# Performance work log

Hardware: AMD Instinct MI355X
Metric: run time of the kernel (lower is better)

The kernel has to match this reference:

```python
import math
import jax, jax.numpy as jnp
import numpy as np

N_HEADS = 8
WINDOW = 4


def _get_relative_embeddings(emb, length, window):
    # emb: [1, 2*window+1, k_channels] -> [1, 2*length-1, k_channels]
    pad_length = max(length - (window + 1), 0)
    start = max(window + 1 - length, 0)
    if pad_length > 0:
        emb = jnp.pad(emb, ((0, 0), (pad_length, pad_length), (0, 0)))
    return emb[:, start:start + 2 * length - 1]


def _relative_position_to_absolute_position(x):
    # x: [b, h, l, 2l-1] -> [b, h, l, l] (skewing trick)
    b, h, l, _ = x.shape
    x = jnp.pad(x, ((0, 0), (0, 0), (0, 0), (0, 1)))
    x_flat = x.reshape(b, h, l * 2 * l)
    x_flat = jnp.pad(x_flat, ((0, 0), (0, 0), (0, l - 1)))
    return x_flat.reshape(b, h, l + 1, 2 * l - 1)[:, :, :l, l - 1:]


def _absolute_position_to_relative_position(x):
    # x: [b, h, l, l] -> [b, h, l, 2l-1]
    b, h, l, _ = x.shape
    x = jnp.pad(x, ((0, 0), (0, 0), (0, 0), (0, l - 1)))
    x_flat = x.reshape(b, h, l * l + l * (l - 1))
    x_flat = jnp.pad(x_flat, ((0, 0), (0, 0), (l, 0)))
    return x_flat.reshape(b, h, l, 2 * l)[:, :, :, 1:]


def setup_inputs() -> dict:
    key = jax.random.key(0)
    ks = jax.random.split(key, 12)
    b, t, d = 4, 1024, 512
    kc = d // N_HEADS
    s = 1.0 / math.sqrt(d)
    return {
        "x": jax.random.normal(ks[0], (b, t, d), jnp.float32),
        "c": jax.random.normal(ks[1], (b, t, d), jnp.float32),
        "wq": jax.random.normal(ks[2], (d, d), jnp.float32) * s,
        "bq": jnp.zeros((d,), jnp.float32),
        "wk": jax.random.normal(ks[3], (d, d), jnp.float32) * s,
        "bk": jnp.zeros((d,), jnp.float32),
        "wv": jax.random.normal(ks[4], (d, d), jnp.float32) * s,
        "bv": jnp.zeros((d,), jnp.float32),
        "wo": jax.random.normal(ks[5], (d, d), jnp.float32) * s,
        "bo": jnp.zeros((d,), jnp.float32),
        "emb_rel_k": jax.random.normal(ks[6], (1, 2 * WINDOW + 1, kc), jnp.float32) * kc ** -0.5,
        "emb_rel_v": jax.random.normal(ks[7], (1, 2 * WINDOW + 1, kc), jnp.float32) * kc ** -0.5,
    }


def reference(x, c, wq, bq, wk, bk, wv, bv, wo, bo, emb_rel_k, emb_rel_v):
    b, t, d = x.shape
    h = N_HEADS
    kc = d // h
    inv_sqrt = 1.0 / math.sqrt(kc)

    # 1x1 conv projections (pointwise matmul)
    q = x @ wq + bq   # [b, t, d]
    k = c @ wk + bk
    v = c @ wv + bv

    # Faithful reshape as in source: [b, t, d] -> [b, h, kc, t] -> [b, h, t, kc]
    q = q.reshape(b, h, kc, t).transpose(0, 1, 3, 2)
    k = k.reshape(b, h, kc, t).transpose(0, 1, 3, 2)
    v = v.reshape(b, h, kc, t).transpose(0, 1, 3, 2)

    scores = jnp.einsum('bhtd,bhsd->bhts', q, k) * inv_sqrt  # [b,h,t,t]

    # relative key logits
    key_rel = _get_relative_embeddings(emb_rel_k, t, WINDOW)[0]  # [2t-1, kc]
    rel_logits = jnp.einsum('bhtd,md->bhtm', q, key_rel)          # [b,h,t,2t-1]
    scores_local = _relative_position_to_absolute_position(rel_logits) * inv_sqrt
    scores = scores + scores_local

    p_attn = jax.nn.softmax(scores, axis=-1)
    output = jnp.einsum('bhts,bhsd->bhtd', p_attn, v)  # [b,h,t,kc]

    # relative value contribution
    rel_weights = _absolute_position_to_relative_position(p_attn)  # [b,h,t,2t-1]
    val_rel = _get_relative_embeddings(emb_rel_v, t, WINDOW)[0]    # [2t-1, kc]
    output = output + jnp.einsum('bhtm,md->bhtd', rel_weights, val_rel)

    # Faithful output reshape: [b,h,t,kc] -> [b,h,kc,t] -> [b,t,d]
    output = output.transpose(0, 1, 3, 2).reshape(b, t, d)
    out = output @ wo + bo
    return out
```

## Files before the change

kernel.cpp:

```cpp
#include <hip/hip_runtime.h>
#include <hip/hip_bf16.h>

#define NB 4
#define NT 1024
#define ND 512
#define NH 8
#define NKC 64

typedef __bf16 bf16x8 __attribute__((ext_vector_type(8)));
typedef float f32x4 __attribute__((ext_vector_type(4)));
typedef unsigned int u32;

__device__ __forceinline__ f32x4 MFMA(bf16x8 a, bf16x8 b, f32x4 c) {
    return __builtin_amdgcn_mfma_f32_16x16x32_bf16(a, b, c, 0, 0, 0);
}
__device__ __forceinline__ unsigned short f2bu(float v) {
    __hip_bfloat16 b = __float2bfloat16(v);
    return *(unsigned short*)&b;
}
__device__ __forceinline__ void split1(float v, unsigned short& h, unsigned short& l)
{
    __hip_bfloat16 hb = __float2bfloat16(v);
    float r = v - __bfloat162float(hb);
    __hip_bfloat16 lb = __float2bfloat16(r);
    h = *(unsigned short*)&hb;
    l = *(unsigned short*)&lb;
}
__device__ __forceinline__ void splitpack(const float4 a, const float4 b, uint4& h, uint4& l)
{
    union { unsigned short u[8]; uint4 v; } H, L;
    const float f[8] = {a.x, a.y, a.z, a.w, b.x, b.y, b.z, b.w};
    #pragma unroll
    for (int j = 0; j < 8; ++j) split1(f[j], H.u[j], L.u[j]);
    h = H.v; l = L.v;
}
__device__ __forceinline__ void gl16(const unsigned short* g, unsigned short* l) {
    __builtin_amdgcn_global_load_lds(
        (const __attribute__((address_space(1))) u32*)g,
        (__attribute__((address_space(3))) u32*)l, 16, 0, 0);
}

__global__ __launch_bounds__(256)
void splitT_kernel(const float* __restrict__ w0, const float* __restrict__ w1,
                   const float* __restrict__ w2, const float* __restrict__ w3,
                   unsigned short* __restrict__ wT)
{
    __shared__ float tl[32][33];
    const float* w = (blockIdx.z == 0) ? w0 : (blockIdx.z == 1) ? w1
                   : (blockIdx.z == 2) ? w2 : w3;
    unsigned short* hi = wT + (size_t)blockIdx.z * 2 * (ND * ND);
    unsigned short* lo = hi + ND * ND;
    const int t = threadIdx.x;
    const int x0 = blockIdx.x * 32, y0 = blockIdx.y * 32;
    {
        const int r = t >> 3, c = (t & 7) * 4;
        const float4 v = *(const float4*)&w[(size_t)(y0 + r) * ND + x0 + c];
        tl[r][c] = v.x; tl[r][c+1] = v.y; tl[r][c+2] = v.z; tl[r][c+3] = v.w;
    }
    __syncthreads();
    {
        const int nr = t >> 3, k4 = (t & 7) * 4;
        unsigned short hh[4], ll[4];
        #pragma unroll
        for (int j = 0; j < 4; ++j) split1(tl[k4 + j][nr], hh[j], ll[j]);
        ushort4 h = make_ushort4(hh[0], hh[1], hh[2], hh[3]);
        ushort4 l = make_ushort4(ll[0], ll[1], ll[2], ll[3]);
        *(ushort4*)&hi[(size_t)(x0 + nr) * ND + y0 + k4] = h;
        *(ushort4*)&lo[(size_t)(x0 + nr) * ND + y0 + k4] = l;
    }
}

__global__ __launch_bounds__(256, 3)
void proj_mfma(const float* __restrict__ x, const float* __restrict__ cc,
               const unsigned short* __restrict__ wT,
               const float* __restrict__ bq, const float* __restrict__ bk,
               const float* __restrict__ bv,
               unsigned short* __restrict__ qh_o, unsigned short* __restrict__ ql_o,
               unsigned short* __restrict__ kh_o, unsigned short* __restrict__ vh_o)
{
    __shared__ unsigned short smem[13312];
    unsigned short* Ah = smem;
    unsigned short* Al = smem + 2560;
    unsigned short* Bh = smem + 5120;
    unsigned short* Bl = smem + 9216;
    unsigned short* Tr = smem;

    const int hw = blockIdx.x + 4 * blockIdx.y + 256 * blockIdx.z;
    const int swz = (hw & 7) * 96 + (hw >> 3);
    const int xt = swz & 3;
    const int yt = (swz >> 2) & 63;
    const int which = swz >> 8;

    const float* A_g = (which == 0) ? x : cc;
    const unsigned short* Bh_g = wT + (size_t)which * 2 * (ND * ND);
    const unsigned short* Bl_g = Bh_g + ND * ND;
    const float* bias = (which == 0) ? bq : (which == 1) ? bk : bv;

    const int tid = threadIdx.x, l = tid & 63, w = tid >> 6;
    const int quad = l >> 4, lc = l & 15;
    const int wm = w & 1, wn = w >> 1;
    const int n0 = xt * 128, m0 = yt * 64;

    const int am = tid >> 2, ak = (tid & 3) * 8;
    const size_t aG = (size_t)(m0 + am) * ND + ak;

    const int lr = l >> 2, lc4 = l & 3;
    const int lcs = lc4 ^ ((lr >> 1) & 3);
    const unsigned short* bsrcH0 = Bh_g + (size_t)(n0 + w * 32 + lr) * ND + lcs * 8;
    const unsigned short* bsrcH1 = bsrcH0 + 16 * ND;
    const unsigned short* bsrcL0 = Bl_g + (size_t)(n0 + w * 32 + lr) * ND + lcs * 8;
    const unsigned short* bsrcL1 = bsrcL0 + 16 * ND;
    unsigned short* bdstH0 = Bh + (w * 32) * 32;
    unsigned short* bdstH1 = Bh + (w * 32 + 16) * 32;
    unsigned short* bdstL0 = Bl + (w * 32) * 32;
    unsigned short* bdstL1 = Bl + (w * 32 + 16) * 32;

    float4 ra0 = *(const float4*)&A_g[aG];
    float4 ra1 = *(const float4*)&A_g[aG + 4];
    uint4 h0, l0;
    splitpack(ra0, ra1, h0, l0);

    const int fsw = (lc >> 1) & 3;
    const int bchunk = (quad ^ fsw) * 8;

    f32x4 acc[2][4];
    #pragma unroll
    for (int mi = 0; mi < 2; ++mi)
        #pragma unroll
        for (int ni = 0; ni < 4; ++ni) acc[mi][ni] = (f32x4){0.f, 0.f, 0.f, 0.f};

    for (int k0 = 0; k0 < ND; k0 += 32) {
        __syncthreads();
        {
            *(uint4*)&Ah[am * 40 + ak] = h0;
            *(uint4*)&Al[am * 40 + ak] = l0;
            gl16(bsrcH0 + k0, bdstH0);
            gl16(bsrcH1 + k0, bdstH1);
            gl16(bsrcL0 + k0, bdstL0);
            gl16(bsrcL1 + k0, bdstL1);
        }
        __syncthreads();
        if (k0 + 32 < ND) {
            const size_t aN = aG + k0 + 32;
            ra0 = *(const float4*)&A_g[aN];
            ra1 = *(const float4*)&A_g[aN + 4];
        }

        bf16x8 ah[2], al2[2], bh[4], bl[4];
        #pragma unroll
        for (int mi = 0; mi < 2; ++mi) {
            const int ar = (wm * 32 + mi * 16 + lc) * 40 + quad * 8;
            ah[mi] = *(const bf16x8*)&Ah[ar];
            al2[mi] = *(const bf16x8*)&Al[ar];
        }
        #pragma unroll
        for (int ni = 0; ni < 4; ++ni) {
            const int br = (wn * 64 + ni * 16 + lc) * 32 + bchunk;
            bh[ni] = *(const bf16x8*)&Bh[br];
            bl[ni] = *(const bf16x8*)&Bl[br];
        }
        #pragma unroll
        for (int mi = 0; mi < 2; ++mi)
            #pragma unroll
            for (int ni = 0; ni < 4; ++ni) {
                acc[mi][ni] = MFMA(al2[mi], bh[ni], acc[mi][ni]);
                acc[mi][ni] = MFMA(ah[mi], bl[ni], acc[mi][ni]);
                acc[mi][ni] = MFMA(ah[mi], bh[ni], acc[mi][ni]);
            }
        if (k0 + 32 < ND) splitpack(ra0, ra1, h0, l0);
    }

    const int bb = m0 >> 10, tt0 = m0 & 1023;
    const int hh = tt0 >> 7, cch0 = (tt0 & 127) >> 1;
    const int bh_idx = bb * NH + hh;

    if (which == 2) {
        #pragma unroll
        for (int ni = 0; ni < 4; ++ni) {
            const int n = n0 + wn * 64 + ni * 16 + lc;
            const float bval = bias[n];
            #pragma unroll
            for (int mi = 0; mi < 2; ++mi)
                #pragma unroll
                for (int r = 0; r < 4; ++r) {
                    const int mloc = wm * 32 + mi * 16 + quad * 4 + r;
                    const int cch = cch0 + (mloc >> 1);
                    const int t = (mloc & 1) * 512 + n;
                    vh_o[(((size_t)bh_idx * 16 + (t >> 6)) * 64 + cch) * 64 + (t & 63)] =
                        f2bu(acc[mi][ni][r] + bval);
                }
        }
        return;
    }

    const int npass = (which == 0) ? 2 : 1;
    unsigned short* outp[2] = {(which == 0) ? qh_o : kh_o, ql_o};

    for (int pass = 0; pass < npass; ++pass) {
        __syncthreads();
        #pragma unroll
        for (int ni = 0; ni < 4; ++ni) {
            const int nloc = wn * 64 + ni * 16 + lc;
            const float bval = bias[n0 + nloc];
            #pragma unroll
            for (int mi = 0; mi < 2; ++mi)
                #pragma unroll
                for (int r = 0; r < 4; ++r) {
                    const int mloc = wm * 32 + mi * 16 + quad * 4 + r;
                    const float val = acc[mi][ni][r] + bval;
                    unsigned short hs, ls;
                    if (which == 0) { split1(val, hs, ls); }
                    else { hs = f2bu(val); ls = 0; }
                    Tr[((mloc & 1) * 128 + nloc) * 40 + (mloc >> 1)] =
                        (pass == 0) ? hs : ls;
                }
        }
        __syncthreads();
        {
            const int t = (tid >> 7) * 512 + n0 + (tid & 127);
            const size_t oa = ((size_t)bh_idx * NT + t) * NKC + cch0;
            const uint4 v0 = *(const uint4*)&Tr[tid * 40];
            const uint4 v1 = *(const uint4*)&Tr[tid * 40 + 8];
            const uint4 v2 = *(const uint4*)&Tr[tid * 40 + 16];
            const uint4 v3 = *(const uint4*)&Tr[tid * 40 + 24];
            *(uint4*)&outp[pass][oa]      = v0;
            *(uint4*)&outp[pass][oa + 8]  = v1;
            *(uint4*)&outp[pass][oa + 16] = v2;
            *(uint4*)&outp[pass][oa + 24] = v3;
        }
    }
}

__global__ __launch_bounds__(256, 4)
void outproj_mfma(const unsigned short* __restrict__ a_g,
                  const unsigned short* __restrict__ wTh,
                  const float* __restrict__ bo, float* __restrict__ out)
{
    __shared__ unsigned short smem2[6144];
    unsigned short* As = smem2;
    unsigned short* Bh = smem2 + 2048;
    unsigned short* Bl = smem2 + 4096;
    const unsigned short* Bl_g = wTh + ND * ND;
    const int tid = threadIdx.x, l = tid & 63, w = tid >> 6;
    const int quad = l >> 4, lc = l & 15;
    const int wm = w & 1, wn = w >> 1;

    const int hw = blockIdx.x + 8 * blockIdx.y;
    const int swz = (hw & 7) * 64 + (hw >> 3);
    const int n0 = (swz & 7) * 64, m0 = (swz >> 3) * 64;

    const int lr = l >> 2, lc4 = l & 3;
    const int lcs = lc4 ^ ((lr >> 1) & 3);
    const unsigned short* asrc  = a_g + (size_t)(m0 + w * 16 + lr) * ND + lcs * 8;
    const unsigned short* bhsrc = wTh + (size_t)(n0 + w * 16 + lr) * ND + lcs * 8;
    const unsigned short* blsrc = Bl_g + (size_t)(n0 + w * 16 + lr) * ND + lcs * 8;
    unsigned short* adst = As + (w * 16) * 32;
    unsigned short* bhdst = Bh + (w * 16) * 32;
    unsigned short* bldst = Bl + (w * 16) * 32;

    const int fsw = (lc >> 1) & 3;
    const int chunk = (quad ^ fsw) * 8;

    f32x4 acc[2][2];
    #pragma unroll
    for (int mi = 0; mi < 2; ++mi)
        #pragma unroll
        for (int ni = 0; ni < 2; ++ni) acc[mi][ni] = (f32x4){0.f, 0.f, 0.f, 0.f};

    for (int k0 = 0; k0 < ND; k0 += 32) {
        __syncthreads();
        gl16(asrc + k0, adst);
        gl16(bhsrc + k0, bhdst);
        gl16(blsrc + k0, bldst);
        __syncthreads();

        bf16x8 ab[2], bhf[2], blf[2];
        #pragma unroll
        for (int mi = 0; mi < 2; ++mi)
            ab[mi] = *(const bf16x8*)&As[(wm * 32 + mi * 16 + lc) * 32 + chunk];
        #pragma unroll
        for (int ni = 0; ni < 2; ++ni) {
            const int br = (wn * 32 + ni * 16 + lc) * 32 + chunk;
            bhf[ni] = *(const bf16x8*)&Bh[br];
            blf[ni] = *(const bf16x8*)&Bl[br];
        }
        #pragma unroll
        for (int mi = 0; mi < 2; ++mi)
            #pragma unroll
            for (int ni = 0; ni < 2; ++ni) {
                acc[mi][ni] = MFMA(ab[mi], bhf[ni], acc[mi][ni]);
                acc[mi][ni] = MFMA(ab[mi], blf[ni], acc[mi][ni]);
            }
    }

    #pragma unroll
    for (int ni = 0; ni < 2; ++ni) {
        const int n = n0 + wn * 32 + ni * 16 + lc;
        const float bval = bo[n];
        #pragma unroll
        for (int mi = 0; mi < 2; ++mi)
            #pragma unroll
            for (int r = 0; r < 4; ++r) {
                const int m = m0 + wm * 32 + mi * 16 + quad * 4 + r;
                out[(size_t)m * ND + n] = acc[mi][ni][r] + bval;
            }
    }
}

__global__ __launch_bounds__(512, 4)
void attn_mfma(const unsigned short* __restrict__ qh_g, const unsigned short* __restrict__ ql_g,
               const unsigned short* __restrict__ kh_g,
               const unsigned short* __restrict__ vh_g,
               const float* __restrict__ embk, const float* __restrict__ embv,
               unsigned short* __restrict__ ath)
{
    __shared__ unsigned short smem[37376];
    unsigned short* KsH = smem;
    unsigned short* Vt  = smem + 9216;
    unsigned short* Ps  = smem + 22528;
    float* bandv = (float*)(smem + 35840);
    unsigned short* EkH = smem + 22528;
    unsigned short* EkL = EkH + 1152;

    const int tid = threadIdx.x, l = tid & 63, w = tid >> 6;
    const int quad = l >> 4, lc = l & 15;
    const int g = w & 3;
    const int h = w >> 2;

    const int hw = blockIdx.x + 16 * blockIdx.y + 128 * blockIdx.z;
    const int swz = (hw & 7) * 64 + (hw >> 3);
    const int q0 = (swz & 15) * 64;
    const int hh = (swz >> 4) & 7, bb = swz >> 7;

    const int sBeg = h * 512;
    const int bh = bb * NH + hh;
    const size_t qkBase = (size_t)bh * NT * NKC;
    const size_t vtBase = (size_t)bh * (16 * 64 * 64);

    unsigned short* KsHg = KsH + h * 4608;
    unsigned short* Vtg  = Vt  + h * 6656;

    const int tl = tid & 255;
    const int srow = tl >> 2, sseg = (tl & 3) * 16;
    uint4 pk0, pk1, pv0, pv1;
    {
        const size_t ka = qkBase + (size_t)(sBeg + srow) * NKC + sseg;
        const size_t va = vtBase + (size_t)(sBeg >> 6) * 4096 + srow * 64 + sseg;
        pk0 = *(const uint4*)&kh_g[ka];
        pk1 = *(const uint4*)&kh_g[ka + 8];
        pv0 = *(const uint4*)&vh_g[va];
        pv1 = *(const uint4*)&vh_g[va + 8];
    }

    for (int idx = tid; idx < 16 * 72; idx += 512) {
        const int d = idx / 72, kc = idx - d * 72;
        const float v = (d < 9 && kc < 64) ? embk[d * 64 + kc] : 0.f;
        unsigned short hs, ls;
        split1(v, hs, ls);
        EkH[idx] = hs;
        EkL[idx] = ls;
    }
    for (int idx = tid; idx < 2 * 64 * 40; idx += 512) {
        const int g2 = idx / 2560, rem = idx - g2 * 2560;
        const int c = rem / 40, d = rem - c * 40;
        Vt[g2 * 6656 + c * 104 + 64 + d] = f2bu((d < 9) ? embv[d * 64 + c] : 0.f);
    }
    __syncthreads();

    bf16x8 qh[2], ql[2];
    {
        const int qg = q0 + g * 16 + lc;
        const size_t qa = qkBase + (size_t)qg * NKC + quad * 8;
        qh[0] = *(const bf16x8*)&qh_g[qa];
        qh[1] = *(const bf16x8*)&qh_g[qa + 32];
        ql[0] = *(const bf16x8*)&ql_g[qa];
        ql[1] = *(const bf16x8*)&ql_g[qa + 32];
    }

    {
        f32x4 accB = (f32x4){0.f, 0.f, 0.f, 0.f};
        #pragma unroll
        for (int kk = 0; kk < 2; ++kk) {
            const bf16x8 ebh = *(const bf16x8*)&EkH[lc * 72 + kk * 32 + quad * 8];
            const bf16x8 ebl = *(const bf16x8*)&EkL[lc * 72 + kk * 32 + quad * 8];
            accB = MFMA(ql[kk], ebh, accB);
            accB = MFMA(qh[kk], ebl, accB);
            accB = MFMA(qh[kk], ebh, accB);
        }
        __syncthreads();
        if (h == 0 && lc <= 8) {
            #pragma unroll
            for (int r = 0; r < 4; ++r)
                bandv[(g * 16 + quad * 4 + r) * 12 + lc] = accB[r];
        }
    }
    unsigned short* P = Ps + w * 1664;
    {
        const int zr = l >> 2, zc = 64 + (l & 3) * 8;
        *(uint4*)&P[zr * 104 + zc] = (uint4){0u, 0u, 0u, 0u};
    }

    f32x4 O[4];
    #pragma unroll
    for (int ci = 0; ci < 4; ++ci) O[ci] = (f32x4){0.f, 0.f, 0.f, 0.f};
    float l_run[4] = {0.f, 0.f, 0.f, 0.f};
    bool prevdiag = false;

    for (int s0 = sBeg; s0 < sBeg + 512; s0 += 64) {
        __syncthreads();
        {
            *(uint4*)&KsHg[srow * 72 + sseg]      = pk0;
            *(uint4*)&KsHg[srow * 72 + sseg + 8]  = pk1;
            *(uint4*)&Vtg[srow * 104 + sseg]      = pv0;
            *(uint4*)&Vtg[srow * 104 + sseg + 8]  = pv1;
        }
        __syncthreads();
        if (s0 + 64 < sBeg + 512) {
            const size_t ka = qkBase + (size_t)(s0 + 64 + srow) * NKC + sseg;
            const size_t va = vtBase + (size_t)((s0 + 64) >> 6) * 4096 + srow * 64 + sseg;
            pk0 = *(const uint4*)&kh_g[ka];
            pk1 = *(const uint4*)&kh_g[ka + 8];
            pv0 = *(const uint4*)&vh_g[va];
            pv1 = *(const uint4*)&vh_g[va + 8];
        }

        const int sd = s0 - q0;
        const bool diag = (sd >= -64) && (sd <= 64);

        f32x4 S[4];
        #pragma unroll
        for (int ni = 0; ni < 4; ++ni) {
            f32x4 a = (f32x4){0.f, 0.f, 0.f, 0.f};
            #pragma unroll
            for (int kk = 0; kk < 2; ++kk) {
                const bf16x8 kb = *(const bf16x8*)&KsHg[(ni * 16 + lc) * 72 + kk * 32 + quad * 8];
                a = MFMA(ql[kk], kb, a);
                a = MFMA(qh[kk], kb, a);
            }
            S[ni] = a;
        }

        if (diag) {
            #pragma unroll
            for (int ni = 0; ni < 4; ++ni)
                #pragma unroll
                for (int r = 0; r < 4; ++r) {
                    const int ql64 = g * 16 + quad * 4 + r;
                    const int dp4 = (s0 + ni * 16 + lc) - (q0 + ql64) + 4;
                    if (dp4 >= 0 && dp4 <= 8) S[ni][r] += bandv[ql64 * 12 + dp4];
                }
        }
        #pragma unroll
        for (int ni = 0; ni < 4; ++ni)
            #pragma unroll
            for (int r = 0; r < 4; ++r)
                S[ni][r] = __expf(S[ni][r] * 0.125f);
        #pragma unroll
        for (int r = 0; r < 4; ++r)
            l_run[r] += S[0][r] + S[1][r] + S[2][r] + S[3][r];

        if (diag || prevdiag) {
            const int zr = l >> 2, zc = 64 + (l & 3) * 4;
            *(ushort4*)&P[zr * 104 + zc] = make_ushort4(0, 0, 0, 0);
        }
        if (diag) {
            #pragma unroll
            for (int ni = 0; ni < 4; ++ni)
                #pragma unroll
                for (int r = 0; r < 4; ++r) {
                    const int prow = quad * 4 + r;
                    const unsigned short pb = f2bu(S[ni][r]);
                    P[prow * 104 + ni * 16 + lc] = pb;
                    const int dp4 = (s0 + ni * 16 + lc) - (q0 + g * 16 + prow) + 4;
                    if (dp4 >= 0 && dp4 <= 8) P[prow * 104 + 64 + dp4] = pb;
                }
        } else {
            #pragma unroll
            for (int ni = 0; ni < 4; ++ni)
                #pragma unroll
                for (int r = 0; r < 4; ++r) {
                    const int prow = quad * 4 + r;
                    P[prow * 104 + ni * 16 + lc] = f2bu(S[ni][r]);
                }
        }

        #pragma unroll
        for (int ks = 0; ks < 3; ++ks) {
            const bf16x8 pa = *(const bf16x8*)&P[lc * 104 + ks * 32 + quad * 8];
            #pragma unroll
            for (int ci = 0; ci < 4; ++ci) {
                const bf16x8 vb = *(const bf16x8*)&Vtg[(ci * 16 + lc) * 104 + ks * 32 + quad * 8];
                O[ci] = MFMA(pa, vb, O[ci]);
            }
        }
        prevdiag = diag;
    }

    #pragma unroll
    for (int r = 0; r < 4; ++r) {
        float v = l_run[r];
        v += __shfl_xor(v, 1); v += __shfl_xor(v, 2);
        v += __shfl_xor(v, 4); v += __shfl_xor(v, 8);
        l_run[r] = v;
    }

    __syncthreads();
    float* Oex = (float*)smem;
    float* l1s = bandv;
    const int qloc0 = g * 16 + quad * 4;

    if (h == 1) {
        #pragma unroll
        for (int ci = 0; ci < 4; ++ci)
            #pragma unroll
            for (int r = 0; r < 4; ++r)
                Oex[(qloc0 + r) * 64 + ci * 16 + lc] = O[ci][r];
        if (lc == 0) {
            #pragma unroll
            for (int r = 0; r < 4; ++r)
                l1s[qloc0 + r] = l_run[r];
        }
    }
    __syncthreads();
    if (h == 0) {
        float linv[4];
        #pragma unroll
        for (int r = 0; r < 4; ++r)
            linv[r] = 1.f / (l_run[r] + l1s[qloc0 + r]);
        #pragma unroll
        for (int ci = 0; ci < 4; ++ci) {
            const int c = ci * 16 + lc;
            const int row = hh * 128 + 2 * c + (q0 >> 9);
            unsigned short o[4];
            #pragma unroll
            for (int r = 0; r < 4; ++r)
                o[r] = f2bu((O[ci][r] + Oex[(qloc0 + r) * 64 + c]) * linv[r]);
            *(ushort4*)&ath[((size_t)bb * NT + row) * ND + (q0 & 511) + qloc0] =
                make_ushort4(o[0], o[1], o[2], o[3]);
        }
    }
}

extern "C" void kernel_launch(void* const* d_in, const int* in_sizes, int n_in,
                              void* d_out, int out_size, void* d_ws, size_t ws_size,
                              hipStream_t stream) {
    const float* x    = (const float*)d_in[0];
    const float* c    = (const float*)d_in[1];
    const float* wq   = (const float*)d_in[2];
    const float* bq   = (const float*)d_in[3];
    const float* wk   = (const float*)d_in[4];
    const float* bk   = (const float*)d_in[5];
    const float* wv   = (const float*)d_in[6];
    const float* bv   = (const float*)d_in[7];
    const float* wo   = (const float*)d_in[8];
    const float* bo   = (const float*)d_in[9];
    const float* embk = (const float*)d_in[10];
    const float* embv = (const float*)d_in[11];

    unsigned short* u16 = (unsigned short*)d_ws;
    const size_t M = 1024 * 1024;
    unsigned short* wT  = u16;
    unsigned short* qh  = u16 + 2 * M;
    unsigned short* ql  = u16 + 4 * M;
    unsigned short* kh  = u16 + 6 * M;
    unsigned short* vh  = u16 + 8 * M;
    unsigned short* ath = u16 + 10 * M;

    splitT_kernel<<<dim3(16, 16, 4), 256, 0, stream>>>(wq, wk, wv, wo, wT);

    proj_mfma<<<dim3(4, 64, 3), 256, 0, stream>>>(x, c, wT, bq, bk, bv,
                                                  qh, ql, kh, vh);

    attn_mfma<<<dim3(16, 8, 4), 512, 0, stream>>>(qh, ql, kh, vh,
                                                  embk, embv, ath);

    outproj_mfma<<<dim3(8, 64), 256, 0, stream>>>(ath,
                                                  wT + (size_t)3 * 2 * ND * ND,
                                                  bo, (float*)d_out);
}
```

Baseline: 150.5 us.

## Load K/V tiles directly into XOR-swizzled LDS and split out value-embedding tile

The register-staged K/V prefetch (global to registers, then registers to padded LDS) becomes direct global-to-LDS 16-byte loads via a gl16 helper, into unpadded tiles with an XOR column swizzle to avoid bank conflicts. The relative value embedding gets its own small shared tile instead of being copied into each V buffer's padding columns, and the third PV MFMA step reads from it. This cuts LDS footprint and register-to-LDS store traffic. The loads are now issued and waited on within the same iteration, so the earlier overlap of next-tile fetch with current compute is lost.

```diff
diff --git a/kernel.cpp b/kernel.cpp
--- a/kernel.cpp
+++ b/kernel.cpp
@@ -314,12 +314,11 @@
                const float* __restrict__ embk, const float* __restrict__ embv,
                unsigned short* __restrict__ ath)
 {
-    __shared__ unsigned short smem[37376];
-    unsigned short* KsH = smem;
-    unsigned short* Vt  = smem + 9216;
-    unsigned short* Ps  = smem + 22528;
-    float* bandv = (float*)(smem + 35840);
-    unsigned short* EkH = smem + 22528;
+    __shared__ unsigned short smem[33792];
+    unsigned short* Ev  = smem + 16384;
+    unsigned short* Ps  = smem + 18944;
+    float* bandv = (float*)(smem + 32256);
+    unsigned short* EkH = smem + 18944;
     unsigned short* EkL = EkH + 1152;
 
     const int tid = threadIdx.x, l = tid & 63, w = tid >> 6;
@@ -337,20 +336,17 @@
     const size_t qkBase = (size_t)bh * NT * NKC;
     const size_t vtBase = (size_t)bh * (16 * 64 * 64);
 
-    unsigned short* KsHg = KsH + h * 4608;
-    unsigned short* Vtg  = Vt  + h * 6656;
+    unsigned short* Ksh = smem + h * 4096;
+    unsigned short* Vsh = smem + 8192 + h * 4096;
 
     const int tl = tid & 255;
-    const int srow = tl >> 2, sseg = (tl & 3) * 16;
-    uint4 pk0, pk1, pv0, pv1;
-    {
-        const size_t ka = qkBase + (size_t)(sBeg + srow) * NKC + sseg;
-        const size_t va = vtBase + (size_t)(sBeg >> 6) * 4096 + srow * 64 + sseg;
-        pk0 = *(const uint4*)&kh_g[ka];
-        pk1 = *(const uint4*)&kh_g[ka + 8];
-        pv0 = *(const uint4*)&vh_g[va];
-        pv1 = *(const uint4*)&vh_g[va + 8];
-    }
+    const int rr = tl >> 3, cc8 = tl & 7;
+    const int cs = cc8 ^ (rr & 7);
+    const unsigned short* kSrc = kh_g + qkBase + (size_t)(sBeg + rr) * NKC + cs * 8;
+    const unsigned short* vSrc = vh_g + vtBase + (size_t)(sBeg >> 6) * 4096 + rr * 64 + cs * 8;
+    const int wvh = tl >> 6;
+    unsigned short* dK = Ksh + wvh * 512;
+    unsigned short* dV = Vsh + wvh * 512;
 
     for (int idx = tid; idx < 16 * 72; idx += 512) {
         const int d = idx / 72, kc = idx - d * 72;
@@ -360,10 +356,9 @@
         EkH[idx] = hs;
         EkL[idx] = ls;
     }
-    for (int idx = tid; idx < 2 * 64 * 40; idx += 512) {
-        const int g2 = idx / 2560, rem = idx - g2 * 2560;
-        const int c = rem / 40, d = rem - c * 40;
-        Vt[g2 * 6656 + c * 104 + 64 + d] = f2bu((d < 9) ? embv[d * 64 + c] : 0.f);
+    for (int idx = tid; idx < 64 * 40; idx += 512) {
+        const int c = idx / 40, d = idx - c * 40;
+        Ev[idx] = f2bu((d < 9) ? embv[d * 64 + c] : 0.f);
     }
     __syncthreads();
 
@@ -400,6 +395,8 @@
         *(uint4*)&P[zr * 104 + zc] = (uint4){0u, 0u, 0u, 0u};
     }
 
+    const int swz8 = lc & 7;
+
     f32x4 O[4];
     #pragma unroll
     for (int ci = 0; ci < 4; ++ci) O[ci] = (f32x4){0.f, 0.f, 0.f, 0.f};
@@ -408,21 +405,10 @@
 
     for (int s0 = sBeg; s0 < sBeg + 512; s0 += 64) {
         __syncthreads();
-        {
-            *(uint4*)&KsHg[srow * 72 + sseg]      = pk0;
-            *(uint4*)&KsHg[srow * 72 + sseg + 8]  = pk1;
-            *(uint4*)&Vtg[srow * 104 + sseg]      = pv0;
-            *(uint4*)&Vtg[srow * 104 + sseg + 8]  = pv1;
-        }
-        __syncthreads();
-        if (s0 + 64 < sBeg + 512) {
-            const size_t ka = qkBase + (size_t)(s0 + 64 + srow) * NKC + sseg;
-            const size_t va = vtBase + (size_t)((s0 + 64) >> 6) * 4096 + srow * 64 + sseg;
-            pk0 = *(const uint4*)&kh_g[ka];
-            pk1 = *(const uint4*)&kh_g[ka + 8];
-            pv0 = *(const uint4*)&vh_g[va];
-            pv1 = *(const uint4*)&vh_g[va + 8];
-        }
+        gl16(kSrc, dK);  gl16(kSrc + 2048, dK + 2048);
+        gl16(vSrc, dV);  gl16(vSrc + 2048, dV + 2048);
+        kSrc += 4096; vSrc += 4096;
+        __syncthreads();
 
         const int sd = s0 - q0;
         const bool diag = (sd >= -64) && (sd <= 64);
@@ -433,7 +419,8 @@
             f32x4 a = (f32x4){0.f, 0.f, 0.f, 0.f};
             #pragma unroll
             for (int kk = 0; kk < 2; ++kk) {
-                const bf16x8 kb = *(const bf16x8*)&KsHg[(ni * 16 + lc) * 72 + kk * 32 + quad * 8];
+                const bf16x8 kb = *(const bf16x8*)
+                    &Ksh[(ni * 16 + lc) * 64 + ((kk * 4 + quad) ^ swz8) * 8];
                 a = MFMA(ql[kk], kb, a);
                 a = MFMA(qh[kk], kb, a);
             }
@@ -485,11 +472,20 @@
         }
 
         #pragma unroll
-        for (int ks = 0; ks < 3; ++ks) {
+        for (int ks = 0; ks < 2; ++ks) {
             const bf16x8 pa = *(const bf16x8*)&P[lc * 104 + ks * 32 + quad * 8];
             #pragma unroll
             for (int ci = 0; ci < 4; ++ci) {
-                const bf16x8 vb = *(const bf16x8*)&Vtg[(ci * 16 + lc) * 104 + ks * 32 + quad * 8];
+                const bf16x8 vb = *(const bf16x8*)
+                    &Vsh[(ci * 16 + lc) * 64 + ((ks * 4 + quad) ^ swz8) * 8];
+                O[ci] = MFMA(pa, vb, O[ci]);
+            }
+        }
+        {
+            const bf16x8 pa = *(const bf16x8*)&P[lc * 104 + 64 + quad * 8];
+            #pragma unroll
+            for (int ci = 0; ci < 4; ++ci) {
+                const bf16x8 vb = *(const bf16x8*)&Ev[(ci * 16 + lc) * 40 + quad * 8];
                 O[ci] = MFMA(pa, vb, O[ci]);
             }
         }
```

New measurement: 149.6 us. About the same (-0.5%).
